# Kernel tuning notes

Measured on AMD Instinct MI355X. Metric: run time of the kernel, lower is better.

Reference implementation:

```python
import math
import jax, jax.numpy as jnp
import numpy as np

B, T, N, D = 8, 12, 512, 64
NN = 16           # neighbors per node
S_FACTOR = 5      # self.s
D_HEAD = 64       # self.d (scaling)
M_SAMPLES = int(S_FACTOR * math.log2(N))  # 45


def _ln(x):
    # LayerNorm over last dim, no affine (elementwise_affine=False)
    mu = jnp.mean(x, axis=-1, keepdims=True)
    var = jnp.var(x, axis=-1, keepdims=True)
    return (x - mu) / jnp.sqrt(var + 1e-5)


def setup_inputs() -> dict:
    key = jax.random.key(0)
    ks = jax.random.split(key, 16)
    w = lambda k, shp: jax.random.normal(k, shp, dtype=jnp.float32) * 0.05
    inp = {
        "x": jax.random.normal(ks[0], (B, T, N, D), dtype=jnp.float32),
        "adj": jax.random.randint(ks[1], (N, NN), 0, N),
        "eigvec": jax.random.normal(ks[2], (D, N, 1), dtype=jnp.float32),
        "eigvalue": jax.random.normal(ks[3], (D,), dtype=jnp.float32),
        "Wq": w(ks[4], (D, D)), "bq": jnp.zeros((D,), jnp.float32),
        "Wk": w(ks[5], (D, D)), "bk": jnp.zeros((D,), jnp.float32),
        "Wv": w(ks[6], (D, D)), "bv": jnp.zeros((D,), jnp.float32),
        "Wo": w(ks[7], (D, D)), "bo": jnp.zeros((D,), jnp.float32),
        "Wp": w(ks[8], (D, 1)), "bp": jnp.zeros((1,), jnp.float32),
        "W1": w(ks[9], (D, D)), "b1": jnp.zeros((D,), jnp.float32),
        "W2": w(ks[10], (D, D)), "b2": jnp.zeros((D,), jnp.float32),
    }
    return inp


def reference(x, adj, eigvec, eigvalue, Wq, bq, Wk, bk, Wv, bv, Wo, bo, Wp, bp, W1, b1, W2, b2):
    # x_ = x + eigvec^T.squeeze(-1) @ diag(eigvalue)  ->  [N,D] broadcast onto [B,T,N,D]
    ev = jnp.squeeze(eigvec, -1).T * eigvalue[None, :]           # [N,D]
    x_ = x + ev
    Q = x_ @ Wq + bq
    K = x_ @ Wk + bk
    V = x_ @ Wv + bv

    # adjacency-gathered GAT sampling
    K_sample = K[:, :, adj, :]                                   # [B,T,N,NN,D]
    V_sample = V[:, :, adj, :]                                   # [B,T,N,NN,D]
    qk = jnp.einsum('btnd,btnkd->btnk', Q, K_sample)             # [B,T,N,NN]
    gat = jnp.einsum('btnk,btnkd->btnd', qk, V_sample)           # [B,T,N,D]
    M = gat @ Wp[:, 0] + bp[0]                                   # [B,T,N]

    # top-k query selection (set is order-invariant downstream)
    _, M_top = jax.lax.top_k(M, M_SAMPLES)                       # [B,T,m]
    Q_red = jnp.take_along_axis(Q, M_top[..., None], axis=2)     # [B,T,m,D]

    scores = jnp.einsum('btmd,btnd->btmn', Q_red, K) / (D_HEAD ** 0.5)
    attn = jax.nn.softmax(scores, axis=-1)                       # [B,T,m,N]

    # argmax-indexed value gather: value[b,t,n] = (attn @ V)[b,t, argmax_m attn[:, n]]
    cp = jnp.argmax(attn, axis=2)                                # [B,T,N]
    av = jnp.einsum('btmn,btnd->btmd', attn, V)                  # [B,T,m,D]
    value = jnp.take_along_axis(av, cp[..., None], axis=2)       # [B,T,N,D]

    value = _ln(value @ Wo + bo + x_)
    h = jax.nn.relu(value @ W1 + b1) @ W2 + b2
    return _ln(h + value)
```

## Files before the change

kernel.cpp:

```cpp
#include <hip/hip_runtime.h>
#include <math.h>

#define Bb 8
#define Tt 12
#define Nn 512
#define Dd 64
#define NNe 16
#define MS 45
#define BT (Bb*Tt)
#define ROWS (BT*Nn)

static __device__ __forceinline__ float bcast_lane(float v, int e) {
    return __uint_as_float(__builtin_amdgcn_readlane(__float_as_uint(v), e));
}

static __device__ __forceinline__ float wave_sum(float v) {
    for (int off = 32; off; off >>= 1) v += __shfl_xor(v, off, 64);
    return v;
}
static __device__ __forceinline__ float wave_max(float v) {
    for (int off = 32; off; off >>= 1) v = fmaxf(v, __shfl_xor(v, off, 64));
    return v;
}

__global__ __launch_bounds__(256) void k_evT(
    const float* __restrict__ eigvec, const float* __restrict__ eigvalue,
    float* __restrict__ evT)
{
    const int i = blockIdx.x * 256 + threadIdx.x;
    const int d = i >> 9, n = i & (Nn - 1);
    evT[n*Dd + d] = eigvec[i] * eigvalue[d];
}

__global__ __launch_bounds__(256) void k_qkv(
    const float* __restrict__ x, const float* __restrict__ evT,
    const float* __restrict__ Wq, const float* __restrict__ bq,
    const float* __restrict__ Wk, const float* __restrict__ bk,
    const float* __restrict__ Wv, const float* __restrict__ bv,
    const float* __restrict__ Wp,
    float* __restrict__ xw, float* __restrict__ Qo,
    float* __restrict__ Ko, float* __restrict__ Vo, float* __restrict__ pv)
{
    __shared__ float sWq[Dd*Dd], sWk[Dd*Dd], sWv[Dd*Dd];
    for (int i = threadIdx.x; i < Dd*Dd; i += 256) {
        sWq[i] = Wq[i]; sWk[i] = Wk[i]; sWv[i] = Wv[i];
    }
    __syncthreads();
    const int wave = threadIdx.x >> 6, lane = threadIdx.x & 63;
    const int base = (blockIdx.x * 4 + wave) * 4;

    float xs[4];
    #pragma unroll
    for (int r = 0; r < 4; ++r) {
        int row = base + r;
        int n = row & (Nn - 1);
        float v = x[(size_t)row*Dd + lane] + evT[n*Dd + lane];
        xs[r] = v;
        xw[(size_t)row*Dd + lane] = v;
    }
    float q[4], k[4], vv[4];
    #pragma unroll
    for (int r = 0; r < 4; ++r) { q[r] = bq[lane]; k[r] = bk[lane]; vv[r] = bv[lane]; }

    for (int e = 0; e < Dd; ++e) {
        float wq = sWq[e*Dd + lane], wk = sWk[e*Dd + lane], wv = sWv[e*Dd + lane];
        #pragma unroll
        for (int r = 0; r < 4; ++r) {
            float xe = bcast_lane(xs[r], e);
            q[r]  += xe * wq;
            k[r]  += xe * wk;
            vv[r] += xe * wv;
        }
    }
    const float wp = Wp[lane];
    #pragma unroll
    for (int r = 0; r < 4; ++r) {
        size_t off = (size_t)(base + r)*Dd + lane;
        Qo[off] = q[r]; Ko[off] = k[r]; Vo[off] = vv[r];
        float p = wave_sum(vv[r] * wp);
        if (lane == 0) pv[base + r] = p;
    }
}

__global__ __launch_bounds__(256) void k_M(
    const float* __restrict__ Q, const float* __restrict__ K,
    const int* __restrict__ adj, const float* __restrict__ pv,
    const float* __restrict__ bp, float* __restrict__ Mout)
{
    __shared__ __attribute__((aligned(16))) float sK[Nn*Dd];
    const int bt = blockIdx.x >> 1;
    const int half = blockIdx.x & 1;

    const float4* Ksrc = reinterpret_cast<const float4*>(K + (size_t)bt*Nn*Dd);
    float4* sK4 = reinterpret_cast<float4*>(sK);
    for (int i4 = threadIdx.x; i4 < Nn*16; i4 += 256) {
        int nn = i4 >> 4, e4 = i4 & 15;
        sK4[(nn << 4) | (e4 ^ (nn & 15))] = Ksrc[i4];
    }
    __syncthreads();

    const int n = half*256 + threadIdx.x;
    float4 q4[16];
    const float4* Qr = reinterpret_cast<const float4*>(Q + ((size_t)bt*Nn + n)*Dd);
    #pragma unroll
    for (int i = 0; i < 16; ++i) q4[i] = Qr[i];

    const float* pvbt = pv + (size_t)bt*Nn;
    float m = bp[0];
    #pragma unroll 1
    for (int k = 0; k < NNe; ++k) {
        const int j = adj[(n << 4) + k];
        const float4* kr = sK4 + ((size_t)j << 4);
        const int sw = j & 15;
        float dot = 0.f;
        #pragma unroll
        for (int e4 = 0; e4 < 16; ++e4) {
            float4 kv = kr[e4 ^ sw];
            dot += q4[e4].x*kv.x + q4[e4].y*kv.y + q4[e4].z*kv.z + q4[e4].w*kv.w;
        }
        m += dot * pvbt[j];
    }
    Mout[bt*Nn + n] = m;
}

__global__ __launch_bounds__(256) void k_topk(
    const float* __restrict__ Mv, int* __restrict__ Mtop)
{
    const int bt = blockIdx.x * 4 + (threadIdx.x >> 6);
    const int lane = threadIdx.x & 63;
    float v[8];
    #pragma unroll
    for (int i = 0; i < 8; ++i) v[i] = Mv[bt*Nn + i*64 + lane];
    for (int s = 0; s < MS; ++s) {
        float bv = v[0]; int bn = lane;
        #pragma unroll
        for (int i = 1; i < 8; ++i) {
            int nn = i*64 + lane;
            if (v[i] > bv) { bv = v[i]; bn = nn; }
        }
        for (int off = 32; off; off >>= 1) {
            float ov = __shfl_xor(bv, off, 64);
            int   on = __shfl_xor(bn, off, 64);
            if (ov > bv || (ov == bv && on < bn)) { bv = ov; bn = on; }
        }
        if (lane == 0) Mtop[bt*MS + s] = bn;
        const int wl = bn & 63, wi = bn >> 6;
        if (lane == wl) {
            #pragma unroll
            for (int i = 0; i < 8; ++i) if (i == wi) v[i] = -INFINITY;
        }
    }
}

__global__ __launch_bounds__(256) void k_scores(
    const float* __restrict__ Q, const float* __restrict__ K,
    const int* __restrict__ Mtop, float* __restrict__ attn)
{
    __shared__ __attribute__((aligned(16))) float sK[Dd*132];
    __shared__ __attribute__((aligned(16))) float sQ[MS*Dd];
    const int bt = blockIdx.x >> 2;
    const int n0 = (blockIdx.x & 3) * 128;
    const float* Kbt = K + (size_t)bt*Nn*Dd;
    const float* Qbt = Q + (size_t)bt*Nn*Dd;
    for (int i = threadIdx.x; i < 128*Dd; i += 256) {
        int nloc = i >> 6, e = i & 63;
        sK[e*132 + nloc] = Kbt[(n0 + nloc)*Dd + e];
    }
    for (int i = threadIdx.x; i < MS*Dd; i += 256) {
        int m = i >> 6, e = i & 63;
        sQ[i] = Qbt[(size_t)Mtop[bt*MS + m]*Dd + e];
    }
    __syncthreads();
    for (int tile = threadIdx.x; tile < 480; tile += 256) {
        const int m0 = (tile >> 5) * 3;
        const int ng = (tile & 31) * 4;
        float ax[3][4] = {};
        for (int e = 0; e < Dd; ++e) {
            const float4 kv = *reinterpret_cast<const float4*>(&sK[e*132 + ng]);
            #pragma unroll
            for (int i = 0; i < 3; ++i) {
                float qv = sQ[(m0 + i)*Dd + e];
                ax[i][0] += qv * kv.x; ax[i][1] += qv * kv.y;
                ax[i][2] += qv * kv.z; ax[i][3] += qv * kv.w;
            }
        }
        #pragma unroll
        for (int i = 0; i < 3; ++i) {
            float4 o;
            o.x = ax[i][0]*0.125f; o.y = ax[i][1]*0.125f;
            o.z = ax[i][2]*0.125f; o.w = ax[i][3]*0.125f;
            *reinterpret_cast<float4*>(
                &attn[((size_t)bt*MS + m0 + i)*Nn + n0 + ng]) = o;
        }
    }
}

__global__ __launch_bounds__(256) void k_softmax(float* __restrict__ attn)
{
    const int gw = blockIdx.x * 4 + (threadIdx.x >> 6);
    const int lane = threadIdx.x & 63;
    if (gw >= BT*MS) return;
    float* row = attn + (size_t)gw*Nn;
    float v[8];
    float mx = -INFINITY;
    #pragma unroll
    for (int i = 0; i < 8; ++i) { v[i] = row[i*64 + lane]; mx = fmaxf(mx, v[i]); }
    mx = wave_max(mx);
    float sum = 0.f;
    #pragma unroll
    for (int i = 0; i < 8; ++i) { v[i] = expf(v[i] - mx); sum += v[i]; }
    sum = wave_sum(sum);
    float inv = 1.f / sum;
    #pragma unroll
    for (int i = 0; i < 8; ++i) row[i*64 + lane] = v[i] * inv;
}

__global__ __launch_bounds__(256) void k_av(
    const float* __restrict__ attn, const float* __restrict__ V,
    float* __restrict__ av)
{
    const int gw = blockIdx.x * 4 + (threadIdx.x >> 6);
    const int lane = threadIdx.x & 63;
    if (gw >= BT*9) return;
    const int bt = gw / 9, m0 = (gw % 9) * 5;
    const float* a0 = attn + ((size_t)bt*MS + m0)*Nn;
    const float* Vbt = V + (size_t)bt*Nn*Dd;
    float acc[5] = {0,0,0,0,0};
    for (int n = 0; n < Nn; ++n) {
        float v = Vbt[n*Dd + lane];
        #pragma unroll
        for (int i = 0; i < 5; ++i) acc[i] += a0[(size_t)i*Nn + n] * v;
    }
    #pragma unroll
    for (int i = 0; i < 5; ++i)
        av[((size_t)bt*MS + m0 + i)*Dd + lane] = acc[i];
}

__global__ __launch_bounds__(256) void k_cp(
    const float* __restrict__ attn, int* __restrict__ cp)
{
    const int t = blockIdx.x * 256 + threadIdx.x;
    const int bt = t >> 9, n = t & (Nn - 1);
    const float* a = attn + (size_t)bt*MS*Nn + n;
    float best = a[0]; int bi = 0;
    for (int m = 1; m < MS; ++m) {
        float v = a[(size_t)m*Nn];
        if (v > best) { best = v; bi = m; }
    }
    cp[t] = bi;
}

__global__ __launch_bounds__(256) void k_final(
    const float* __restrict__ av, const int* __restrict__ cp,
    const float* __restrict__ xw,
    const float* __restrict__ Wo, const float* __restrict__ bo,
    const float* __restrict__ W1, const float* __restrict__ b1,
    const float* __restrict__ W2, const float* __restrict__ b2,
    float* __restrict__ out)
{
    __shared__ float sWo[Dd*Dd], sW1[Dd*Dd], sW2[Dd*Dd];
    for (int i = threadIdx.x; i < Dd*Dd; i += 256) {
        sWo[i] = Wo[i]; sW1[i] = W1[i]; sW2[i] = W2[i];
    }
    __syncthreads();
    const int wave = threadIdx.x >> 6, lane = threadIdx.x & 63;
    const int base = (blockIdx.x * 4 + wave) * 4;
    const int bt = base >> 9;

    float g[4], o[4];
    #pragma unroll
    for (int r = 0; r < 4; ++r) {
        int c = cp[base + r];
        g[r] = av[((size_t)bt*MS + c)*Dd + lane];
        o[r] = bo[lane] + xw[(size_t)(base + r)*Dd + lane];
    }
    for (int e = 0; e < Dd; ++e) {
        float w = sWo[e*Dd + lane];
        #pragma unroll
        for (int r = 0; r < 4; ++r) o[r] += bcast_lane(g[r], e) * w;
    }
    float val[4];
    #pragma unroll
    for (int r = 0; r < 4; ++r) {
        float mu = wave_sum(o[r]) * (1.f/64.f);
        float d  = o[r] - mu;
        float vs = wave_sum(d*d) * (1.f/64.f);
        val[r] = d * rsqrtf(vs + 1e-5f);
    }
    float u[4];
    #pragma unroll
    for (int r = 0; r < 4; ++r) u[r] = b1[lane];
    for (int e = 0; e < Dd; ++e) {
        float w = sW1[e*Dd + lane];
        #pragma unroll
        for (int r = 0; r < 4; ++r) u[r] += bcast_lane(val[r], e) * w;
    }
    #pragma unroll
    for (int r = 0; r < 4; ++r) u[r] = fmaxf(u[r], 0.f);
    float h[4];
    #pragma unroll
    for (int r = 0; r < 4; ++r) h[r] = b2[lane];
    for (int e = 0; e < Dd; ++e) {
        float w = sW2[e*Dd + lane];
        #pragma unroll
        for (int r = 0; r < 4; ++r) h[r] += bcast_lane(u[r], e) * w;
    }
    #pragma unroll
    for (int r = 0; r < 4; ++r) {
        float x2 = h[r] + val[r];
        float mu = wave_sum(x2) * (1.f/64.f);
        float d  = x2 - mu;
        float vs = wave_sum(d*d) * (1.f/64.f);
        out[(size_t)(base + r)*Dd + lane] = d * rsqrtf(vs + 1e-5f);
    }
}

extern "C" void kernel_launch(void* const* d_in, const int* in_sizes, int n_in,
                              void* d_out, int out_size, void* d_ws, size_t ws_size,
                              hipStream_t stream)
{
    const float* x        = (const float*)d_in[0];
    const int*   adj      = (const int*)  d_in[1];
    const float* eigvec   = (const float*)d_in[2];
    const float* eigvalue = (const float*)d_in[3];
    const float* Wq = (const float*)d_in[4],  *bq = (const float*)d_in[5];
    const float* Wk = (const float*)d_in[6],  *bk = (const float*)d_in[7];
    const float* Wv = (const float*)d_in[8],  *bv = (const float*)d_in[9];
    const float* Wo = (const float*)d_in[10], *bo = (const float*)d_in[11];
    const float* Wp = (const float*)d_in[12], *bp = (const float*)d_in[13];
    const float* W1 = (const float*)d_in[14], *b1 = (const float*)d_in[15];
    const float* W2 = (const float*)d_in[16], *b2 = (const float*)d_in[17];

    const size_t RD = (size_t)ROWS * Dd;
    float* ws   = (float*)d_ws;
    float* Q    = ws;
    float* K    = Q + RD;
    float* V    = K + RD;
    float* Mv   = V + RD;
    float* attn = Mv + ROWS;
    float* av   = attn + (size_t)BT*MS*Nn;
    float* pv   = av + (size_t)BT*MS*Dd;
    float* evT  = pv + ROWS;
    int*   Mtop = (int*)(evT + Nn*Dd);
    int*   cp   = Mtop + BT*MS;
    float* xw   = (float*)d_out;
    float* out  = (float*)d_out;

    k_evT   <<<(Dd*Nn)/256, 256, 0, stream>>>(eigvec, eigvalue, evT);
    k_qkv   <<<ROWS/16, 256, 0, stream>>>(x, evT, Wq,bq, Wk,bk, Wv,bv, Wp, xw, Q, K, V, pv);
    k_M     <<<BT*2,    256, 0, stream>>>(Q, K, adj, pv, bp, Mv);
    k_topk  <<<BT/4,    256, 0, stream>>>(Mv, Mtop);
    k_scores<<<BT*4,    256, 0, stream>>>(Q, K, Mtop, attn);
    k_softmax<<<(BT*MS)/4, 256, 0, stream>>>(attn);
    k_av    <<<(BT*9)/4, 256, 0, stream>>>(attn, V, av);
    k_cp    <<<ROWS/256, 256, 0, stream>>>(attn, cp);
    k_final <<<ROWS/16, 256, 0, stream>>>(av, cp, xw, Wo,bo, W1,b1, W2,b2, out);
}
```

Measured before the change: 273.3 us.

## Drop xw round-trip, double rows per wave, reuse one shared weight buffer

```diff
diff --git a/kernel.cpp b/kernel.cpp
--- a/kernel.cpp
+++ b/kernel.cpp
@@ -13,7 +13,6 @@
 static __device__ __forceinline__ float bcast_lane(float v, int e) {
     return __uint_as_float(__builtin_amdgcn_readlane(__float_as_uint(v), e));
 }
-
 static __device__ __forceinline__ float wave_sum(float v) {
     for (int off = 32; off; off >>= 1) v += __shfl_xor(v, off, 64);
     return v;
@@ -38,34 +37,42 @@
     const float* __restrict__ Wk, const float* __restrict__ bk,
     const float* __restrict__ Wv, const float* __restrict__ bv,
     const float* __restrict__ Wp,
-    float* __restrict__ xw, float* __restrict__ Qo,
-    float* __restrict__ Ko, float* __restrict__ Vo, float* __restrict__ pv)
-{
-    __shared__ float sWq[Dd*Dd], sWk[Dd*Dd], sWv[Dd*Dd];
-    for (int i = threadIdx.x; i < Dd*Dd; i += 256) {
-        sWq[i] = Wq[i]; sWk[i] = Wk[i]; sWv[i] = Wv[i];
+    float* __restrict__ Qo, float* __restrict__ Ko,
+    float* __restrict__ Vo, float* __restrict__ pv)
+{
+    __shared__ __attribute__((aligned(16))) float sWq[Dd*Dd], sWk[Dd*Dd], sWv[Dd*Dd];
+    {
+        const float4* a = reinterpret_cast<const float4*>(Wq);
+        const float4* b = reinterpret_cast<const float4*>(Wk);
+        const float4* c = reinterpret_cast<const float4*>(Wv);
+        float4* sa = reinterpret_cast<float4*>(sWq);
+        float4* sb = reinterpret_cast<float4*>(sWk);
+        float4* sc = reinterpret_cast<float4*>(sWv);
+        #pragma unroll
+        for (int i = 0; i < 4; ++i) {
+            sa[i*256 + threadIdx.x] = a[i*256 + threadIdx.x];
+            sb[i*256 + threadIdx.x] = b[i*256 + threadIdx.x];
+            sc[i*256 + threadIdx.x] = c[i*256 + threadIdx.x];
+        }
     }
     __syncthreads();
     const int wave = threadIdx.x >> 6, lane = threadIdx.x & 63;
-    const int base = (blockIdx.x * 4 + wave) * 4;
-
-    float xs[4];
-    #pragma unroll
-    for (int r = 0; r < 4; ++r) {
-        int row = base + r;
-        int n = row & (Nn - 1);
-        float v = x[(size_t)row*Dd + lane] + evT[n*Dd + lane];
-        xs[r] = v;
-        xw[(size_t)row*Dd + lane] = v;
-    }
-    float q[4], k[4], vv[4];
-    #pragma unroll
-    for (int r = 0; r < 4; ++r) { q[r] = bq[lane]; k[r] = bk[lane]; vv[r] = bv[lane]; }
+    const int base = blockIdx.x * 32 + wave * 8;
+
+    float xs[8];
+    #pragma unroll
+    for (int r = 0; r < 8; ++r) {
+        int row = base + r, n = row & (Nn - 1);
+        xs[r] = x[(size_t)row*Dd + lane] + evT[n*Dd + lane];
+    }
+    float q[8], k[8], vv[8];
+    #pragma unroll
+    for (int r = 0; r < 8; ++r) { q[r] = bq[lane]; k[r] = bk[lane]; vv[r] = bv[lane]; }
 
     for (int e = 0; e < Dd; ++e) {
         float wq = sWq[e*Dd + lane], wk = sWk[e*Dd + lane], wv = sWv[e*Dd + lane];
         #pragma unroll
-        for (int r = 0; r < 4; ++r) {
+        for (int r = 0; r < 8; ++r) {
             float xe = bcast_lane(xs[r], e);
             q[r]  += xe * wq;
             k[r]  += xe * wk;
@@ -74,7 +81,7 @@
     }
     const float wp = Wp[lane];
     #pragma unroll
-    for (int r = 0; r < 4; ++r) {
+    for (int r = 0; r < 8; ++r) {
         size_t off = (size_t)(base + r)*Dd + lane;
         Qo[off] = q[r]; Ko[off] = k[r]; Vo[off] = vv[r];
         float p = wave_sum(vv[r] * wp);
@@ -252,61 +259,77 @@
 
 __global__ __launch_bounds__(256) void k_final(
     const float* __restrict__ av, const int* __restrict__ cp,
-    const float* __restrict__ xw,
+    const float* __restrict__ x, const float* __restrict__ evT,
     const float* __restrict__ Wo, const float* __restrict__ bo,
     const float* __restrict__ W1, const float* __restrict__ b1,
     const float* __restrict__ W2, const float* __restrict__ b2,
     float* __restrict__ out)
 {
-    __shared__ float sWo[Dd*Dd], sW1[Dd*Dd], sW2[Dd*Dd];
-    for (int i = threadIdx.x; i < Dd*Dd; i += 256) {
-        sWo[i] = Wo[i]; sW1[i] = W1[i]; sW2[i] = W2[i];
-    }
-    __syncthreads();
+    __shared__ __attribute__((aligned(16))) float sW[Dd*Dd];
     const int wave = threadIdx.x >> 6, lane = threadIdx.x & 63;
-    const int base = (blockIdx.x * 4 + wave) * 4;
+    const int base = blockIdx.x * 32 + wave * 8;
     const int bt = base >> 9;
 
-    float g[4], o[4];
-    #pragma unroll
-    for (int r = 0; r < 4; ++r) {
-        int c = cp[base + r];
+    const float4* Wo4 = reinterpret_cast<const float4*>(Wo);
+    const float4* W14 = reinterpret_cast<const float4*>(W1);
+    const float4* W24 = reinterpret_cast<const float4*>(W2);
+    float4* sW4 = reinterpret_cast<float4*>(sW);
+
+    float g[8], o[8];
+    #pragma unroll
+    for (int r = 0; r < 8; ++r) {
+        int row = base + r, n = row & (Nn - 1);
+        int c = cp[row];
         g[r] = av[((size_t)bt*MS + c)*Dd + lane];
-        o[r] = bo[lane] + xw[(size_t)(base + r)*Dd + lane];
-    }
+        o[r] = bo[lane] + x[(size_t)row*Dd + lane] + evT[n*Dd + lane];
+    }
+    #pragma unroll
+    for (int i = 0; i < 4; ++i) sW4[i*256 + threadIdx.x] = Wo4[i*256 + threadIdx.x];
+    __syncthreads();
+
     for (int e = 0; e < Dd; ++e) {
-        float w = sWo[e*Dd + lane];
-        #pragma unroll
-        for (int r = 0; r < 4; ++r) o[r] += bcast_lane(g[r], e) * w;
-    }
-    float val[4];
-    #pragma unroll
-    for (int r = 0; r < 4; ++r) {
+        float w = sW[e*Dd + lane];
+        #pragma unroll
+        for (int r = 0; r < 8; ++r) o[r] += bcast_lane(g[r], e) * w;
+    }
+    float val[8];
+    #pragma unroll
+    for (int r = 0; r < 8; ++r) {
         float mu = wave_sum(o[r]) * (1.f/64.f);
         float d  = o[r] - mu;
         float vs = wave_sum(d*d) * (1.f/64.f);
         val[r] = d * rsqrtf(vs + 1e-5f);
     }
-    float u[4];
-    #pragma unroll
-    for (int r = 0; r < 4; ++r) u[r] = b1[lane];
+    __syncthreads();
+    #pragma unroll
+    for (int i = 0; i < 4; ++i) sW4[i*256 + threadIdx.x] = W14[i*256 + threadIdx.x];
+    __syncthreads();
+
+    float u[8];
+    #pragma unroll
+    for (int r = 0; r < 8; ++r) u[r] = b1[lane];
     for (int e = 0; e < Dd; ++e) {
-        float w = sW1[e*Dd + lane];
-        #pragma unroll
-        for (int r = 0; r < 4; ++r) u[r] += bcast_lane(val[r], e) * w;
-    }
-    #pragma unroll
-    for (int r = 0; r < 4; ++r) u[r] = fmaxf(u[r], 0.f);
-    float h[4];
-    #pragma unroll
-    for (int r = 0; r < 4; ++r) h[r] = b2[lane];
+        float w = sW[e*Dd + lane];
+        #pragma unroll
+        for (int r = 0; r < 8; ++r) u[r] += bcast_lane(val[r], e) * w;
+    }
+    #pragma unroll
+    for (int r = 0; r < 8; ++r) u[r] = fmaxf(u[r], 0.f);
+    __syncthreads();
+    #pragma unroll
+    for (int i = 0; i < 4; ++i) sW4[i*256 + threadIdx.x] = W24[i*256 + threadIdx.x];
+    __syncthreads();
+
+    float h[8];
+    #pragma unroll
+    for (int r = 0; r < 8; ++r) h[r] = b2[lane];
     for (int e = 0; e < Dd; ++e) {
-        float w = sW2[e*Dd + lane];
-        #pragma unroll
-        for (int r = 0; r < 4; ++r) h[r] += bcast_lane(u[r], e) * w;
-    }
-    #pragma unroll
-    for (int r = 0; r < 4; ++r) {
+        float w = sW[e*Dd + lane];
+        #pragma unroll
+        for (int r = 0; r < 8; ++r) h[r] += bcast_lane(u[r], e) * w;
+    }
+    #pragma unroll
+    for (int r = 0; r < 8; ++r) {
         float x2 = h[r] + val[r];
         float mu = wave_sum(x2) * (1.f/64.f);
         float d  = x2 - mu;
@@ -343,16 +366,15 @@
     float* evT  = pv + ROWS;
     int*   Mtop = (int*)(evT + Nn*Dd);
     int*   cp   = Mtop + BT*MS;
-    float* xw   = (float*)d_out;
     float* out  = (float*)d_out;
 
     k_evT   <<<(Dd*Nn)/256, 256, 0, stream>>>(eigvec, eigvalue, evT);
-    k_qkv   <<<ROWS/16, 256, 0, stream>>>(x, evT, Wq,bq, Wk,bk, Wv,bv, Wp, xw, Q, K, V, pv);
+    k_qkv   <<<ROWS/32, 256, 0, stream>>>(x, evT, Wq,bq, Wk,bk, Wv,bv, Wp, Q, K, V, pv);
     k_M     <<<BT*2,    256, 0, stream>>>(Q, K, adj, pv, bp, Mv);
     k_topk  <<<BT/4,    256, 0, stream>>>(Mv, Mtop);
     k_scores<<<BT*4,    256, 0, stream>>>(Q, K, Mtop, attn);
     k_softmax<<<(BT*MS)/4, 256, 0, stream>>>(attn);
     k_av    <<<(BT*9)/4, 256, 0, stream>>>(attn, V, av);
     k_cp    <<<ROWS/256, 256, 0, stream>>>(attn, cp);
-    k_final <<<ROWS/16, 256, 0, stream>>>(av, cp, xw, Wo,bo, W1,b1, W2,b2, out);
-}
+    k_final <<<ROWS/32, 256, 0, stream>>>(av, cp, x, evT, Wo,bo, W1,b1, W2,b2, out);
+}
```

Measured after the change: 278.6 us. No clear change (+1.9%).
